# Optimization experiments

Measured on AMD Instinct MI355X. Metric: run time of the kernel, lower is better.

Reference implementation:

```python
import jax, jax.numpy as jnp
import numpy as np

def setup_inputs() -> dict:
    key = jax.random.key(0)
    k1, k2, k3, k4 = jax.random.split(key, 4)
    B, T, C, D = 4, 4096, 1024, 128
    x = jax.random.normal(k1, (B, T, C), dtype=jnp.float32)
    Wq = jax.random.normal(k2, (C, D), dtype=jnp.float32) * (C ** -0.5)
    Wk = jax.random.normal(k3, (C, D), dtype=jnp.float32) * (C ** -0.5)
    Wv = jax.random.normal(k4, (C, D), dtype=jnp.float32) * (C ** -0.5)
    return {"x": x, "Wq": Wq, "Wk": Wk, "Wv": Wv}

def reference(x, Wq, Wk, Wv):
    # x: [B,T,C]; Wq/Wk/Wv: [C,D] (nn.Linear bias=False => x @ W)
    B, T, C = x.shape
    q = jnp.einsum('btc,cd->btd', x, Wq)  # [B,T,D]
    k = jnp.einsum('btc,cd->btd', x, Wk)
    v = jnp.einsum('btc,cd->btd', x, Wv)
    dk = q.shape[-1]
    scale = dk ** -0.5
    w = jnp.einsum('btd,bsd->bts', q, k) * scale  # [B,T,T]
    causal = jnp.tril(jnp.ones((T, T), dtype=bool))
    w = jnp.where(causal, w, -jnp.inf)
    w = jax.nn.softmax(w, axis=-1)
    # dropout p=0.0 => identity
    attention = jnp.einsum('bts,bsd->btd', w, v)  # [B,T,D]
    return attention
```

## Files before the change

### kernel.cpp

```cpp
#include <hip/hip_runtime.h>
#include <stdint.h>

typedef __bf16 bf16_t;
typedef bf16_t bf16x8 __attribute__((ext_vector_type(8)));
typedef float f32x4 __attribute__((ext_vector_type(4)));
typedef float f32x16 __attribute__((ext_vector_type(16)));
typedef unsigned short us8 __attribute__((ext_vector_type(8)));
typedef unsigned short us4 __attribute__((ext_vector_type(4)));
typedef unsigned int u32x4 __attribute__((ext_vector_type(4)));

#define B_ 4
#define T_ 4096
#define C_ 1024
#define D_ 128

#define NCHUNK_PB 144
#define QSCALE 0.12751744f
#define M0 14.0f

__device__ __forceinline__ uint16_t f2bf(float f) {
    union { float f; uint32_t u; } v; v.f = f;
    uint32_t u = v.u;
    uint32_t r = (u + 0x7fffu + ((u >> 16) & 1u)) >> 16;
    return (uint16_t)r;
}

__device__ __forceinline__ uint16_t bfru(float f) {
    return (uint16_t)((__float_as_uint(f) + 0x8000u) >> 16);
}

__device__ __forceinline__ float bf2f(uint16_t u) {
    return __uint_as_float((uint32_t)u << 16);
}

__device__ __forceinline__ uint32_t cvtpk(float a, float b) {
    uint32_t r;
    asm("v_cvt_pk_bf16_f32 %0, %1, %2" : "=v"(r) : "v"(a), "v"(b));
    return r;
}

__device__ __forceinline__ void pl32swap(uint32_t& a, uint32_t& b) {
    asm("v_permlane32_swap_b32 %0, %1" : "+v"(a), "+v"(b));
}

__device__ __forceinline__ void gload_lds16(const void* g, void* l) {
    __builtin_amdgcn_global_load_lds(
        (const __attribute__((address_space(1))) void*)g,
        (__attribute__((address_space(3))) void*)l, 16, 0, 0);
}

__global__ __launch_bounds__(256) void prep_w(const float* __restrict__ Wq,
                                              const float* __restrict__ Wk,
                                              const float* __restrict__ Wv,
                                              uint16_t* __restrict__ WT) {
    int idx = blockIdx.x * 256 + threadIdx.x;
    if (idx >= 3 * D_ * C_) return;
    int w   = idx / (D_ * C_);
    int rem = idx - w * (D_ * C_);
    int n   = rem / C_;
    int k   = rem - n * C_;
    const float* W = (w == 0) ? Wq : (w == 1) ? Wk : Wv;
    WT[idx] = f2bf(W[(size_t)k * D_ + n]);
}

__global__ __launch_bounds__(512, 2) void qkv_fused(const float* __restrict__ x,
                                                    const uint16_t* __restrict__ WT,
                                                    uint16_t* __restrict__ qb,
                                                    uint16_t* __restrict__ kb,
                                                    uint16_t* __restrict__ vT) {
    __shared__ __align__(16) float    A_lds[2][64 * 32];
    __shared__ __align__(16) uint16_t W_lds[2][192 * 64];

    int tid  = threadIdx.x;
    int lane = tid & 63;
    int wave = tid >> 6;
    int quad = lane >> 4;
    int lx   = lane & 15;
    int wm   = wave >> 2;
    int wn   = wave & 3;

    int m0 = blockIdx.x * 64;

    auto issue_ab = [&](int bi, int k0) {
        {
            int row = wave * 8 + (lane >> 3);
            int gch = (lane & 7) ^ (row & 7);
            gload_lds16(x + (size_t)(m0 + row) * C_ + k0 + gch * 4,
                        &A_lds[bi][(wave * 8) * 32]);
        }
#pragma unroll
        for (int c = 0; c < 3; c++) {
            int fl  = wave * 24 + c * 8 + (lane >> 3);
            int gch = (lane & 7) ^ (fl & 7);
            int wsel = fl >> 6;
            int n    = 2 * (fl & 63) + (gch >> 2);
            gload_lds16(WT + (size_t)wsel * (D_ * C_) + (size_t)n * C_ + k0 + (gch & 3) * 8,
                        &W_lds[bi][(wave * 24 + c * 8) * 64]);
        }
    };

    f32x4 acc[3][2][2];
#pragma unroll
    for (int w = 0; w < 3; w++)
#pragma unroll
        for (int mf = 0; mf < 2; mf++)
#pragma unroll
            for (int nf = 0; nf < 2; nf++)
                acc[w][mf][nf] = (f32x4){0.f, 0.f, 0.f, 0.f};

    issue_ab(0, 0);
    int cur = 0;

    for (int k0 = 0; k0 < C_; k0 += 32) {
        __syncthreads();
        if (k0 + 32 < C_) issue_ab(cur ^ 1, k0 + 32);

        bf16x8 af[2];
#pragma unroll
        for (int mf = 0; mf < 2; mf++) {
            int arow = wm * 32 + mf * 16 + lx;
            const float* ar = &A_lds[cur][arow * 32];
            f32x4 a0 = *(const f32x4*)&ar[((2 * quad) ^ (arow & 7)) * 4];
            f32x4 a1 = *(const f32x4*)&ar[((2 * quad + 1) ^ (arow & 7)) * 4];
            u32x4 w = (u32x4){cvtpk(a0[0], a0[1]), cvtpk(a0[2], a0[3]),
                              cvtpk(a1[0], a1[1]), cvtpk(a1[2], a1[3])};
            af[mf] = *(bf16x8*)&w;
        }

#pragma unroll
        for (int wsel = 0; wsel < 3; wsel++)
#pragma unroll
            for (int nf = 0; nf < 2; nf++) {
                int n  = wn * 32 + nf * 16 + lx;
                int rp = n >> 1;
                int ch = ((n & 1) * 4 + quad) ^ (rp & 7);
                bf16x8 wf = *(const bf16x8*)&W_lds[cur][(wsel * 64 + rp) * 64 + ch * 8];
                acc[wsel][0][nf] = __builtin_amdgcn_mfma_f32_16x16x32_bf16(af[0], wf, acc[wsel][0][nf], 0, 0, 0);
                acc[wsel][1][nf] = __builtin_amdgcn_mfma_f32_16x16x32_bf16(af[1], wf, acc[wsel][1][nf], 0, 0, 0);
            }
        cur ^= 1;
    }

#pragma unroll
    for (int mf = 0; mf < 2; mf++) {
        int mrow0 = m0 + wm * 32 + mf * 16 + quad * 4;
        int batch = mrow0 >> 12;
        int t     = mrow0 & 4095;
#pragma unroll
        for (int nf = 0; nf < 2; nf++) {
            int n = wn * 32 + nf * 16 + lx;
#pragma unroll
            for (int r = 0; r < 4; r++) {
                qb[(size_t)(mrow0 + r) * D_ + n] = bfru(acc[0][mf][nf][r] * QSCALE);
                kb[(size_t)(mrow0 + r) * D_ + n] = bfru(acc[1][mf][nf][r]);
            }
            us4 pv;
#pragma unroll
            for (int r = 0; r < 4; r++) pv[r] = bfru(acc[2][mf][nf][r]);
            *(us4*)&vT[(size_t)batch * D_ * T_ + (size_t)n * T_ + t] = pv;
        }
    }
}

__global__ __launch_bounds__(256, 2) void attn(const uint16_t* __restrict__ qb,
                                               const uint16_t* __restrict__ kb,
                                               const uint16_t* __restrict__ vT,
                                               uint16_t* __restrict__ part,
                                               float* __restrict__ ml) {
    __shared__ __align__(16) uint16_t K_lds[2][64 * 128];
    __shared__ __align__(16) uint16_t V_lds[2][128 * 64];

    int tid  = threadIdx.x;
    int lane = tid & 63;
    int wave = tid >> 6;
    int q31  = lane & 31;
    int hi   = lane >> 5;

    int batch = blockIdx.x & 3;
    int L     = NCHUNK_PB - 1 - (blockIdx.x >> 2);
    int a = 0;
    while (a < 7 && 2 * (a + 1) * (a + 2) <= L) a++;
    int rem   = L - 2 * a * (a + 1);
    int jt    = 4 * a + rem / (a + 1);
    int chunk = rem - (rem / (a + 1)) * (a + 1);
    int lidx  = batch * NCHUNK_PB + L;

    int q0     = jt * 128;
    int st0    = chunk * 8;
    int ntiles = min(8, 2 * jt + 2 - st0);

    auto issue_kv = [&](int bi, int tile) {
        int s0i = tile * 64;
        const uint16_t* kB = kb + (size_t)(batch * T_ + s0i) * D_;
#pragma unroll
        for (int j = 0; j < 4; j++) {
            int row = wave * 16 + j * 4 + (lane >> 4);
            int gch = (lane & 15) ^ (row & 7);
            gload_lds16(kB + (size_t)row * D_ + gch * 8,
                        &K_lds[bi][(wave * 16 + j * 4) * 128]);
        }
        const uint16_t* vB = vT + (size_t)batch * D_ * T_ + s0i;
#pragma unroll
        for (int j = 0; j < 4; j++) {
            int row = wave * 32 + j * 8 + (lane >> 3);
            int gch = (lane & 7) ^ (row & 7);
            gload_lds16(vB + (size_t)row * T_ + gch * 8,
                        &V_lds[bi][(wave * 32 + j * 8) * 64]);
        }
    };

    bf16x8 qf[8];
    {
        const uint16_t* qp = qb + (size_t)(batch * T_ + q0 + wave * 32 + q31) * D_ + hi * 8;
#pragma unroll
        for (int kc = 0; kc < 8; kc++) qf[kc] = *(const bf16x8*)(qp + kc * 16);
    }

    f32x16 o[4];
#pragma unroll
    for (int i = 0; i < 4; i++)
#pragma unroll
        for (int r = 0; r < 16; r++) o[i][r] = 0.f;
    float lsum = 0.f;

    issue_kv(0, st0);
    int cur = 0;

    for (int it = 0; it < ntiles; it++) {
        int s0 = (st0 + it) * 64;
        __syncthreads();
        if (it + 1 < ntiles) issue_kv(cur ^ 1, st0 + it + 1);

        f32x16 st[2];
#pragma unroll
        for (int nt = 0; nt < 2; nt++)
#pragma unroll
            for (int r = 0; r < 16; r++) st[nt][r] = 0.f;
        __builtin_amdgcn_s_setprio(1);
#pragma unroll
        for (int kc = 0; kc < 8; kc++)
#pragma unroll
            for (int nt = 0; nt < 2; nt++) {
                int row = nt * 32 + q31;
                bf16x8 kf = *(const bf16x8*)&K_lds[cur][row * 128 + (((kc * 2 + hi) ^ (row & 7)) * 8)];
                st[nt] = __builtin_amdgcn_mfma_f32_32x32x16_bf16(kf, qf[kc], st[nt], 0, 0, 0);
            }
        __builtin_amdgcn_s_setprio(0);

        if (st0 + it >= 2 * jt) {
            int qg = q0 + wave * 32 + q31;
#pragma unroll
            for (int nt = 0; nt < 2; nt++)
#pragma unroll
                for (int r = 0; r < 16; r++) {
                    int sg = s0 + nt * 32 + (r & 3) + 8 * (r >> 2) + 4 * hi;
                    if (sg > qg) st[nt][r] = -INFINITY;
                }
        }

#pragma unroll
        for (int nt = 0; nt < 2; nt++)
#pragma unroll
            for (int r = 0; r < 16; r++) {
                st[nt][r] = exp2f(st[nt][r] - M0);
                lsum += st[nt][r];
            }

        bf16x8 pa[4];
#pragma unroll
        for (int nt = 0; nt < 2; nt++) {
            uint32_t x0 = cvtpk(st[nt][0],  st[nt][1]);
            uint32_t x1 = cvtpk(st[nt][2],  st[nt][3]);
            uint32_t y0 = cvtpk(st[nt][4],  st[nt][5]);
            uint32_t y1 = cvtpk(st[nt][6],  st[nt][7]);
            pl32swap(x0, y0);
            pl32swap(x1, y1);
            u32x4 w0 = (u32x4){x0, x1, y0, y1};
            pa[2 * nt] = *(bf16x8*)&w0;
            uint32_t z0 = cvtpk(st[nt][8],  st[nt][9]);
            uint32_t z1 = cvtpk(st[nt][10], st[nt][11]);
            uint32_t t0 = cvtpk(st[nt][12], st[nt][13]);
            uint32_t t1 = cvtpk(st[nt][14], st[nt][15]);
            pl32swap(z0, t0);
            pl32swap(z1, t1);
            u32x4 w1 = (u32x4){z0, z1, t0, t1};
            pa[2 * nt + 1] = *(bf16x8*)&w1;
        }

        __builtin_amdgcn_s_setprio(1);
#pragma unroll
        for (int sb = 0; sb < 4; sb++)
#pragma unroll
            for (int ntd = 0; ntd < 4; ntd++) {
                int row = ntd * 32 + q31;
                bf16x8 vf = *(const bf16x8*)&V_lds[cur][row * 64 + (((sb * 2 + hi) ^ (row & 7)) * 8)];
                o[ntd] = __builtin_amdgcn_mfma_f32_32x32x16_bf16(pa[sb], vf, o[ntd], 0, 0, 0);
            }
        __builtin_amdgcn_s_setprio(0);
        cur ^= 1;
    }

    lsum += __shfl_xor(lsum, 32, 64);

    uint16_t* pp = part + (size_t)lidx * (128 * 128);
#pragma unroll
    for (int ntd = 0; ntd < 4; ntd++)
#pragma unroll
        for (int r = 0; r < 16; r++) {
            int lrow = wave * 32 + (r & 3) + 8 * (r >> 2) + 4 * hi;
            pp[lrow * 128 + ntd * 32 + q31] = bfru(o[ntd][r]);
        }
    if (lane < 32)
        ml[(size_t)lidx * 128 + wave * 32 + q31] = lsum;
}

__global__ __launch_bounds__(256) void combine(const uint16_t* __restrict__ part,
                                               const float* __restrict__ ml,
                                               float* __restrict__ out) {
    int bidx  = blockIdx.x;
    int half  = bidx & 1;
    int jt    = (bidx >> 1) & 31;
    int batch = bidx >> 6;
    int a     = jt >> 2;
    int base  = batch * NCHUNK_PB + 2 * a * (a + 1) + (jt - 4 * a) * (a + 1);
    int nch   = a + 1;

    int tid  = threadIdx.x;
    int lrow = tid >> 1;
    int c0   = half * 64 + (tid & 1) * 32;

    float Lsum = 0.f;
    f32x4 acc[8];
#pragma unroll
    for (int i = 0; i < 8; i++) acc[i] = (f32x4){0.f, 0.f, 0.f, 0.f};

    for (int c = 0; c < nch; c++) {
        Lsum += ml[(size_t)(base + c) * 128 + lrow];
        const uint16_t* p = part + (size_t)(base + c) * (128 * 128) + lrow * 128 + c0;
#pragma unroll
        for (int i = 0; i < 4; i++) {
            us8 v = *(const us8*)(p + i * 8);
#pragma unroll
            for (int j = 0; j < 8; j++)
                acc[i * 2 + (j >> 2)][j & 3] += bf2f(v[j]);
        }
    }
    float inv = 1.f / Lsum;
    size_t row = (size_t)(batch * T_ + jt * 128 + lrow);
#pragma unroll
    for (int i = 0; i < 8; i++)
        *(f32x4*)(out + row * 128 + c0 + i * 4) = acc[i] * inv;
}

extern "C" void kernel_launch(void* const* d_in, const int* in_sizes, int n_in,
                              void* d_out, int out_size, void* d_ws, size_t ws_size,
                              hipStream_t stream) {
    const float* x  = (const float*)d_in[0];
    const float* Wq = (const float*)d_in[1];
    const float* Wk = (const float*)d_in[2];
    const float* Wv = (const float*)d_in[3];
    float* out = (float*)d_out;

    uint16_t* ws = (uint16_t*)d_ws;
    uint16_t* qb = ws;
    uint16_t* kb = qb + (size_t)16384 * 128;
    uint16_t* vT = kb + (size_t)16384 * 128;
    uint16_t* WT = vT + (size_t)16384 * 128;
    uint16_t* part = WT + (size_t)3 * D_ * C_;
    float* ml = (float*)(part + (size_t)4 * NCHUNK_PB * 128 * 128);

    prep_w<<<dim3((3 * D_ * C_ + 255) / 256), dim3(256), 0, stream>>>(Wq, Wk, Wv, WT);
    qkv_fused<<<dim3(16384 / 64), dim3(512), 0, stream>>>(x, WT, qb, kb, vT);
    attn<<<dim3(B_ * NCHUNK_PB), dim3(256), 0, stream>>>(qb, kb, vT, part, ml);
    combine<<<dim3(B_ * 32 * 2), dim3(256), 0, stream>>>(part, ml, out);
}
```

Baseline: 186.3 us.

## Split fused QKV projection into per-weight blocks to raise grid parallelism

The QKV projection kernel now launches three blocks per 64-row tile (one each for Q, K, V) with 256 threads instead of one 512-thread block computing all three. This gives 768 blocks rather than 256 so more CUs are busy, and the W tile in LDS shrinks, which allows higher occupancy. The cost is that each x tile is loaded and converted to bf16 three times, tripling fp32 activation reads from global memory.

```diff
diff --git a/kernel.cpp b/kernel.cpp
--- a/kernel.cpp
+++ b/kernel.cpp
@@ -63,50 +63,52 @@
     WT[idx] = f2bf(W[(size_t)k * D_ + n]);
 }
 
-__global__ __launch_bounds__(512, 2) void qkv_fused(const float* __restrict__ x,
+__global__ __launch_bounds__(256, 3) void qkv_split(const float* __restrict__ x,
                                                     const uint16_t* __restrict__ WT,
                                                     uint16_t* __restrict__ qb,
                                                     uint16_t* __restrict__ kb,
                                                     uint16_t* __restrict__ vT) {
     __shared__ __align__(16) float    A_lds[2][64 * 32];
-    __shared__ __align__(16) uint16_t W_lds[2][192 * 64];
+    __shared__ __align__(16) uint16_t W_lds[2][128 * 32];
 
     int tid  = threadIdx.x;
     int lane = tid & 63;
     int wave = tid >> 6;
     int quad = lane >> 4;
     int lx   = lane & 15;
-    int wm   = wave >> 2;
-    int wn   = wave & 3;
-
-    int m0 = blockIdx.x * 64;
+    int wm   = wave >> 1;
+    int wn   = wave & 1;
+
+    int bx   = blockIdx.x;
+    int wsel = bx >> 8;
+    int m0   = (bx & 255) * 64;
+    const uint16_t* Wp = WT + (size_t)wsel * (D_ * C_);
 
     auto issue_ab = [&](int bi, int k0) {
-        {
-            int row = wave * 8 + (lane >> 3);
-            int gch = (lane & 7) ^ (row & 7);
+#pragma unroll
+        for (int j = 0; j < 2; j++) {
+            int rbase = wave * 16 + j * 8;
+            int row   = rbase + (lane >> 3);
+            int gch   = (lane & 7) ^ (row & 7);
             gload_lds16(x + (size_t)(m0 + row) * C_ + k0 + gch * 4,
-                        &A_lds[bi][(wave * 8) * 32]);
-        }
-#pragma unroll
-        for (int c = 0; c < 3; c++) {
-            int fl  = wave * 24 + c * 8 + (lane >> 3);
-            int gch = (lane & 7) ^ (fl & 7);
-            int wsel = fl >> 6;
-            int n    = 2 * (fl & 63) + (gch >> 2);
-            gload_lds16(WT + (size_t)wsel * (D_ * C_) + (size_t)n * C_ + k0 + (gch & 3) * 8,
-                        &W_lds[bi][(wave * 24 + c * 8) * 64]);
+                        &A_lds[bi][rbase * 32]);
+        }
+#pragma unroll
+        for (int j = 0; j < 2; j++) {
+            int rbase = wave * 32 + j * 16;
+            int row   = rbase + (lane >> 2);
+            int gch   = (lane & 3) ^ ((row >> 1) & 3);
+            gload_lds16(Wp + (size_t)row * C_ + k0 + gch * 8,
+                        &W_lds[bi][rbase * 32]);
         }
     };
 
-    f32x4 acc[3][2][2];
-#pragma unroll
-    for (int w = 0; w < 3; w++)
-#pragma unroll
-        for (int mf = 0; mf < 2; mf++)
-#pragma unroll
-            for (int nf = 0; nf < 2; nf++)
-                acc[w][mf][nf] = (f32x4){0.f, 0.f, 0.f, 0.f};
+    f32x4 acc[2][4];
+#pragma unroll
+    for (int mf = 0; mf < 2; mf++)
+#pragma unroll
+        for (int nf = 0; nf < 4; nf++)
+            acc[mf][nf] = (f32x4){0.f, 0.f, 0.f, 0.f};
 
     issue_ab(0, 0);
     int cur = 0;
@@ -128,16 +130,12 @@
         }
 
 #pragma unroll
-        for (int wsel = 0; wsel < 3; wsel++)
-#pragma unroll
-            for (int nf = 0; nf < 2; nf++) {
-                int n  = wn * 32 + nf * 16 + lx;
-                int rp = n >> 1;
-                int ch = ((n & 1) * 4 + quad) ^ (rp & 7);
-                bf16x8 wf = *(const bf16x8*)&W_lds[cur][(wsel * 64 + rp) * 64 + ch * 8];
-                acc[wsel][0][nf] = __builtin_amdgcn_mfma_f32_16x16x32_bf16(af[0], wf, acc[wsel][0][nf], 0, 0, 0);
-                acc[wsel][1][nf] = __builtin_amdgcn_mfma_f32_16x16x32_bf16(af[1], wf, acc[wsel][1][nf], 0, 0, 0);
-            }
+        for (int nf = 0; nf < 4; nf++) {
+            int n = wn * 64 + nf * 16 + lx;
+            bf16x8 wf = *(const bf16x8*)&W_lds[cur][n * 32 + ((quad ^ ((n >> 1) & 3)) * 8)];
+            acc[0][nf] = __builtin_amdgcn_mfma_f32_16x16x32_bf16(af[0], wf, acc[0][nf], 0, 0, 0);
+            acc[1][nf] = __builtin_amdgcn_mfma_f32_16x16x32_bf16(af[1], wf, acc[1][nf], 0, 0, 0);
+        }
         cur ^= 1;
     }
 
@@ -147,17 +145,22 @@
         int batch = mrow0 >> 12;
         int t     = mrow0 & 4095;
 #pragma unroll
-        for (int nf = 0; nf < 2; nf++) {
-            int n = wn * 32 + nf * 16 + lx;
-#pragma unroll
-            for (int r = 0; r < 4; r++) {
-                qb[(size_t)(mrow0 + r) * D_ + n] = bfru(acc[0][mf][nf][r] * QSCALE);
-                kb[(size_t)(mrow0 + r) * D_ + n] = bfru(acc[1][mf][nf][r]);
+        for (int nf = 0; nf < 4; nf++) {
+            int n = wn * 64 + nf * 16 + lx;
+            if (wsel == 0) {
+#pragma unroll
+                for (int r = 0; r < 4; r++)
+                    qb[(size_t)(mrow0 + r) * D_ + n] = bfru(acc[mf][nf][r] * QSCALE);
+            } else if (wsel == 1) {
+#pragma unroll
+                for (int r = 0; r < 4; r++)
+                    kb[(size_t)(mrow0 + r) * D_ + n] = bfru(acc[mf][nf][r]);
+            } else {
+                us4 pv;
+#pragma unroll
+                for (int r = 0; r < 4; r++) pv[r] = bfru(acc[mf][nf][r]);
+                *(us4*)&vT[(size_t)batch * D_ * T_ + (size_t)n * T_ + t] = pv;
             }
-            us4 pv;
-#pragma unroll
-            for (int r = 0; r < 4; r++) pv[r] = bfru(acc[2][mf][nf][r]);
-            *(us4*)&vT[(size_t)batch * D_ * T_ + (size_t)n * T_ + t] = pv;
         }
     }
 }
@@ -370,7 +373,7 @@
     float* ml = (float*)(part + (size_t)4 * NCHUNK_PB * 128 * 128);
 
     prep_w<<<dim3((3 * D_ * C_ + 255) / 256), dim3(256), 0, stream>>>(Wq, Wk, Wv, WT);
-    qkv_fused<<<dim3(16384 / 64), dim3(512), 0, stream>>>(x, WT, qb, kb, vT);
+    qkv_split<<<dim3(3 * 256), dim3(256), 0, stream>>>(x, WT, qb, kb, vT);
     attn<<<dim3(B_ * NCHUNK_PB), dim3(256), 0, stream>>>(qb, kb, vT, part, ml);
     combine<<<dim3(B_ * 32 * 2), dim3(256), 0, stream>>>(part, ml, out);
 }
```

Result: faster. 181.5 us (-2.6%).
